# Optimization experiments

Hardware: AMD Instinct MI355X
Metric: run time of the kernel (lower is better)

## Reference

```python
import jax, jax.numpy as jnp
import numpy as np

N_NODES = 50000
N_EDGES = 1600000
IN_DIM = 6
H = 64


def _sage_conv(x, src, dst, W_l, b_l, W_r, num_nodes):
    """PyG SAGEConv (aggr='mean'): out = lin_l(mean_{j in N(i)} x_j) + lin_r(x_i).
    lin_l has bias, lin_r has no bias (PyG default)."""
    # mean-aggregate neighbor features at destination nodes
    agg = jax.ops.segment_sum(x[src], dst, num_segments=num_nodes)          # [N, d]
    cnt = jax.ops.segment_sum(jnp.ones((src.shape[0],), x.dtype), dst,
                              num_segments=num_nodes)                        # [N]
    mean = agg / jnp.maximum(cnt, 1.0)[:, None]
    return mean @ W_l + b_l + x @ W_r


def setup_inputs() -> dict:
    key = jax.random.key(0)
    ks = jax.random.split(key, 8)
    x = jax.random.normal(ks[0], (N_NODES, IN_DIM), dtype=jnp.float32)
    edge_index = jax.random.randint(ks[1], (2, N_EDGES), 0, N_NODES, dtype=jnp.int64)
    # Kaiming-ish scaled params
    def lin(k, fan_in, fan_out):
        return jax.random.normal(k, (fan_in, fan_out), dtype=jnp.float32) / np.sqrt(fan_in)
    return {
        "x": x,
        "edge_index": edge_index,
        "W1_l": lin(ks[2], IN_DIM, H),
        "b1_l": jnp.zeros((H,), jnp.float32),
        "W1_r": lin(ks[3], IN_DIM, H),
        "W2_l": lin(ks[4], H, H),
        "b2_l": jnp.zeros((H,), jnp.float32),
        "W2_r": lin(ks[5], H, H),
    }


def reference(x, edge_index, W1_l, b1_l, W1_r, W2_l, b2_l, W2_r):
    src, dst = edge_index[0], edge_index[1]
    n = x.shape[0]
    z = jax.nn.relu(_sage_conv(x, src, dst, W1_l, b1_l, W1_r, n))  # [N, H]
    z = _sage_conv(z, src, dst, W2_l, b2_l, W2_r, n)               # [N, H]
    return z
```

## Files before the change

### kernel.cpp

```cpp
#include <hip/hip_runtime.h>

#define N_NODES 50000
#define N_EDGES 1600000
#define IN_DIM 6
#define H 64

#define NBUCKET 196
#define NBLK 196
#define EPB 8192
#define BCAP 9216

#define L2PAD 72

__device__ __forceinline__ float bf2f(unsigned short u) {
    return __uint_as_float(((unsigned int)u) << 16);
}
__device__ __forceinline__ unsigned short f2bf(float f) {
    unsigned int u = __float_as_uint(f);
    u += 0x7fffu + ((u >> 16) & 1u);
    return (unsigned short)(u >> 16);
}

__global__ __launch_bounds__(512) void scatter_bucketed(
        const int* __restrict__ ei,
        const float* __restrict__ x,
        int* __restrict__ gcur,
        unsigned int* __restrict__ ebin,
        const float* __restrict__ W2l,
        const float* __restrict__ W2r,
        unsigned short* __restrict__ Wlt,
        unsigned short* __restrict__ Wrt,
        unsigned short* __restrict__ z,
        float* __restrict__ xp) {
    int t = threadIdx.x;
    int gid = blockIdx.x * 512 + t;
    if (gid < N_NODES) {
        const float2* xr = (const float2*)(x + (size_t)gid * IN_DIM);
        float2 p0 = xr[0], p1 = xr[1], p2 = xr[2];
        float4* xw = (float4*)(xp + ((size_t)gid << 3));
        xw[0] = make_float4(p0.x, p0.y, p1.x, p1.y);
        xw[1] = make_float4(p2.x, p2.y, 0.f, 0.f);
    }
    if (blockIdx.x == NBLK) {
        for (int i = t; i < H * H; i += 512) {
            int k = i >> 6, f = i & 63;
            Wlt[f * H + k] = f2bf(W2l[i]);
            Wrt[f * H + k] = f2bf(W2r[i]);
        }
        if (t < H) z[(size_t)N_NODES * H + t] = 0;
        return;
    }
    __shared__ unsigned int sedge[EPB];
    __shared__ int hist[NBUCKET];
    __shared__ int cur[NBUCKET];
    for (int i = t; i < NBUCKET; i += 512) hist[i] = 0;
    __syncthreads();
    int e0 = blockIdx.x * EPB;
    int cnt = min(EPB, N_EDGES - e0);
    const int4* s4 = (const int4*)(ei + e0);
    const int4* d4 = (const int4*)(ei + N_EDGES + e0);
    for (int k = t; k * 4 < cnt; k += 512) {
        int4 sv = s4[k];
        int4 dv = d4[k];
        sedge[k * 4 + 0] = ((unsigned)sv.x << 16) | (unsigned)dv.x;
        sedge[k * 4 + 1] = ((unsigned)sv.y << 16) | (unsigned)dv.y;
        sedge[k * 4 + 2] = ((unsigned)sv.z << 16) | (unsigned)dv.z;
        sedge[k * 4 + 3] = ((unsigned)sv.w << 16) | (unsigned)dv.w;
        atomicAdd(&hist[dv.x >> 8], 1);
        atomicAdd(&hist[dv.y >> 8], 1);
        atomicAdd(&hist[dv.z >> 8], 1);
        atomicAdd(&hist[dv.w >> 8], 1);
    }
    __syncthreads();
    for (int i = t; i < NBUCKET; i += 512)
        cur[i] = atomicAdd(&gcur[i], hist[i]);
    __syncthreads();
    for (int k = t; k * 4 < cnt; k += 512) {
#pragma unroll
        for (int j = 0; j < 4; j++) {
            unsigned int p = sedge[k * 4 + j];
            int b = (int)(p & 0xffffu) >> 8;
            int pos = atomicAdd(&cur[b], 1);
            if (pos < BCAP) ebin[(size_t)b * BCAP + pos] = p;
        }
    }
}

__global__ __launch_bounds__(1024) void bucket_layer1(
        const unsigned int* __restrict__ ebin,
        const int* __restrict__ gcur,
        const float* __restrict__ xp,
        const float* __restrict__ W1l,
        const float* __restrict__ b1,
        const float* __restrict__ W1r,
        int2* __restrict__ rowpair,
        unsigned short* __restrict__ esrc,
        unsigned short* __restrict__ z) {
    __shared__ int raw[BCAP];
    __shared__ unsigned short ssrc[BCAP];
    __shared__ int sdeg[256];
    __shared__ int sstart[256];
    __shared__ int scur[256];
    __shared__ int wsum[4];
    __shared__ float sW1l[IN_DIM * H];
    __shared__ float sW1r[IN_DIM * H];
    float* smx   = (float*)raw;
    float* spart = (float*)raw + 4096;

    int t = threadIdx.x;
    int lane = t & 63, w = t >> 6;
    int b = blockIdx.x;
    int base = b << 8;
    int nn = min(256, N_NODES - base);
    int ebase = b * BCAP;
    int cnt = min(gcur[b], BCAP);

    if (t < 256) sdeg[t] = 0;
    if (t < IN_DIM * H) { sW1l[t] = W1l[t]; sW1r[t] = W1r[t]; }
    for (int i = t; i < cnt; i += 1024) raw[i] = (int)ebin[ebase + i];
    __syncthreads();
    for (int i = t; i < cnt; i += 1024) atomicAdd(&sdeg[raw[i] & 0xff], 1);
    __syncthreads();
    int v = 0, s = 0;
    if (t < 256) {
        v = sdeg[t]; s = v;
#pragma unroll
        for (int off = 1; off < 64; off <<= 1) {
            int u = __shfl_up(s, off);
            if (lane >= off) s += u;
        }
        if (lane == 63) wsum[w] = s;
    }
    __syncthreads();
    if (t < 256) {
        int woff = 0;
        for (int k = 0; k < w; k++) woff += wsum[k];
        int excl = s - v + woff;
        sstart[t] = excl;
        scur[t] = excl;
        if (t < nn) rowpair[base + t] = make_int2(ebase + excl, ebase + excl + v);
    }
    __syncthreads();
    for (int i = t; i < cnt; i += 1024) {
        int p = raw[i];
        int pos = atomicAdd(&scur[p & 0xff], 1);
        ssrc[pos] = (unsigned short)((unsigned)p >> 16);
    }
    __syncthreads();
    for (int i = t; i < cnt; i += 1024)
        esrc[ebase + i] = ssrc[i];
    for (int i = t; i < nn * 8; i += 1024) {
        int node = i >> 3, k = i & 7;
        if (k < 6) smx[node * 16 + 6 + k] = xp[(size_t)(base + node) * 8 + k];
    }

    int node = t & 255, q = t >> 8;
    float a0 = 0.f, a1 = 0.f, a2 = 0.f, a3 = 0.f, a4 = 0.f, a5 = 0.f;
    int deg = 0, st = 0;
    if (node < nn) { deg = sdeg[node]; st = sstart[node]; }
    for (int i = st + q; i < st + deg; i += 4) {
        int src = ssrc[i];
        const float4* xs = (const float4*)(xp + ((size_t)src << 3));
        float4 p0 = xs[0], p1 = xs[1];
        a0 += p0.x; a1 += p0.y; a2 += p0.z;
        a3 += p0.w; a4 += p1.x; a5 += p1.y;
    }
    if (q > 0 && node < nn) {
        float* sp = &spart[(q - 1) * (256 * 6) + node * 6];
        sp[0] = a0; sp[1] = a1; sp[2] = a2; sp[3] = a3; sp[4] = a4; sp[5] = a5;
    }
    __syncthreads();
    if (q == 0 && node < nn) {
        float inv = 1.0f / fmaxf((float)deg, 1.0f);
        const float* p1p = &spart[0 * (256 * 6) + node * 6];
        const float* p2p = &spart[1 * (256 * 6) + node * 6];
        const float* p3p = &spart[2 * (256 * 6) + node * 6];
        smx[node * 16 + 0] = (a0 + p1p[0] + p2p[0] + p3p[0]) * inv;
        smx[node * 16 + 1] = (a1 + p1p[1] + p2p[1] + p3p[1]) * inv;
        smx[node * 16 + 2] = (a2 + p1p[2] + p2p[2] + p3p[2]) * inv;
        smx[node * 16 + 3] = (a3 + p1p[3] + p2p[3] + p3p[3]) * inv;
        smx[node * 16 + 4] = (a4 + p1p[4] + p2p[4] + p3p[4]) * inv;
        smx[node * 16 + 5] = (a5 + p1p[5] + p2p[5] + p3p[5]) * inv;
    }
    __syncthreads();

    int feat = t & 63, ng = t >> 6;
    float wl[IN_DIM], wr[IN_DIM];
#pragma unroll
    for (int k = 0; k < IN_DIM; k++) { wl[k] = sW1l[k * H + feat]; wr[k] = sW1r[k * H + feat]; }
    float bias = b1[feat];
    for (int nb = ng; nb < nn; nb += 16) {
        const float4* row = (const float4*)&smx[nb * 16];
        float4 r0 = row[0], r1 = row[1], r2 = row[2];
        float acc = bias;
        acc += r0.x * wl[0] + r0.y * wl[1] + r0.z * wl[2]
             + r0.w * wl[3] + r1.x * wl[4] + r1.y * wl[5];
        acc += r1.z * wr[0] + r1.w * wr[1] + r2.x * wr[2]
             + r2.y * wr[3] + r2.z * wr[4] + r2.w * wr[5];
        z[(size_t)(base + nb) * H + feat] = f2bf(fmaxf(acc, 0.0f));
    }
}

__global__ __launch_bounds__(512) void layer2_mfma(
        const unsigned short* __restrict__ zin,
        const int2* __restrict__ rowpair,
        const unsigned short* __restrict__ esrc,
        const unsigned short* __restrict__ Wlt,
        const float* __restrict__ b2,
        const unsigned short* __restrict__ Wrt,
        float* __restrict__ out) {
    typedef short bf16x8 __attribute__((ext_vector_type(8)));
    typedef float f32x4 __attribute__((ext_vector_type(4)));
    __shared__ __attribute__((aligned(16))) unsigned short smean[32 * L2PAD];
    __shared__ __attribute__((aligned(16))) unsigned short szl[32 * L2PAD];
    __shared__ __attribute__((aligned(16))) unsigned short sWl[64 * L2PAD];
    __shared__ __attribute__((aligned(16))) unsigned short sWr[64 * L2PAD];

    int t = threadIdx.x;
    int w = t >> 6, lane = t & 63;
    int g = lane >> 4, lg = lane & 15;
    int n0 = blockIdx.x * 32;

    {
        const ushort4* wl4 = (const ushort4*)Wlt;
        const ushort4* wr4 = (const ushort4*)Wrt;
        for (int qi = t; qi < H * H / 4; qi += 512) {
            int f = qi >> 4, kq = qi & 15;
            *(ushort4*)&sWl[f * L2PAD + kq * 4] = wl4[qi];
            *(ushort4*)&sWr[f * L2PAD + kq * 4] = wr4[qi];
        }
    }

    for (int q = 0; q < 4; q++) {
        int ln = w * 4 + q;
        int n = n0 + ln;
        bool valid = (n < N_NODES);
        int r0 = 0, r1 = 0;
        if (valid) { int2 rp = rowpair[n]; r0 = rp.x; r1 = rp.y; }
        float4 acc = make_float4(0.f, 0.f, 0.f, 0.f);
        for (int base = r0; base < r1; base += 64) {
            int ii = base + lane;
            int idx = (ii < r1) ? (int)esrc[ii] : N_NODES;
            int rem = r1 - base;
#pragma unroll
            for (int tt = 0; tt < 8; tt++) {
                int s = __shfl(idx, tt * 4 + g);
                const ushort4* zr = (const ushort4*)(zin + (size_t)s * H);
                ushort4 vv = zr[lg];
                acc.x += bf2f(vv.x); acc.y += bf2f(vv.y);
                acc.z += bf2f(vv.z); acc.w += bf2f(vv.w);
            }
            if (rem > 32) {
#pragma unroll
                for (int tt = 8; tt < 16; tt++) {
                    int s = __shfl(idx, tt * 4 + g);
                    const ushort4* zr = (const ushort4*)(zin + (size_t)s * H);
                    ushort4 vv = zr[lg];
                    acc.x += bf2f(vv.x); acc.y += bf2f(vv.y);
                    acc.z += bf2f(vv.z); acc.w += bf2f(vv.w);
                }
            }
        }
#pragma unroll
        for (int off = 16; off < 64; off <<= 1) {
            acc.x += __shfl_xor(acc.x, off);
            acc.y += __shfl_xor(acc.y, off);
            acc.z += __shfl_xor(acc.z, off);
            acc.w += __shfl_xor(acc.w, off);
        }
        float inv = 1.0f / fmaxf((float)(r1 - r0), 1.0f);
        if (g == 0) {
            ushort4 mb;
            mb.x = f2bf(acc.x * inv); mb.y = f2bf(acc.y * inv);
            mb.z = f2bf(acc.z * inv); mb.w = f2bf(acc.w * inv);
            *(ushort4*)&smean[ln * L2PAD + lg * 4] = mb;
        }
        int nz = valid ? n : N_NODES;
        szl[ln * L2PAD + lane] = zin[(size_t)nz * H + lane];
    }
    __syncthreads();

    int nb = w >> 2, fb = w & 3;
    f32x4 acc = {0.f, 0.f, 0.f, 0.f};
#pragma unroll
    for (int ks = 0; ks < 2; ks++) {
        int ko = ks * 32 + g * 8;
        bf16x8 aM = *(const bf16x8*)&smean[(nb * 16 + lg) * L2PAD + ko];
        bf16x8 aZ = *(const bf16x8*)&szl[(nb * 16 + lg) * L2PAD + ko];
        bf16x8 bL = *(const bf16x8*)&sWl[(fb * 16 + lg) * L2PAD + ko];
        bf16x8 bR = *(const bf16x8*)&sWr[(fb * 16 + lg) * L2PAD + ko];
        acc = __builtin_amdgcn_mfma_f32_16x16x32_bf16(aM, bL, acc, 0, 0, 0);
        acc = __builtin_amdgcn_mfma_f32_16x16x32_bf16(aZ, bR, acc, 0, 0, 0);
    }
    float bias = b2[fb * 16 + lg];
#pragma unroll
    for (int r = 0; r < 4; r++) {
        int node = n0 + nb * 16 + g * 4 + r;
        if (node < N_NODES)
            out[(size_t)node * H + fb * 16 + lg] = acc[r] + bias;
    }
}

extern "C" void kernel_launch(void* const* d_in, const int* in_sizes, int n_in,
                              void* d_out, int out_size, void* d_ws, size_t ws_size,
                              hipStream_t stream) {
    const float* x   = (const float*)d_in[0];
    const int*   ei  = (const int*)d_in[1];
    const float* W1l = (const float*)d_in[2];
    const float* b1  = (const float*)d_in[3];
    const float* W1r = (const float*)d_in[4];
    const float* W2l = (const float*)d_in[5];
    const float* b2  = (const float*)d_in[6];
    const float* W2r = (const float*)d_in[7];
    float* out = (float*)d_out;

    int* gcur = (int*)d_ws;
    int2* rowpair = (int2*)(gcur + 208);
    unsigned int*   ebin = (unsigned int*)(rowpair + N_NODES);
    unsigned short* esrc = (unsigned short*)(ebin + (size_t)NBUCKET * BCAP);
    unsigned short* z    = esrc + (size_t)NBUCKET * BCAP;
    unsigned short* Wlt  = z + (size_t)(N_NODES + 1) * H;
    unsigned short* Wrt  = Wlt + H * H;
    float* xp = (float*)(Wrt + H * H);

    hipMemsetAsync(gcur, 0, NBUCKET * sizeof(int), stream);

    scatter_bucketed<<<NBLK + 1, 512, 0, stream>>>(ei, x, gcur, ebin,
                                                   W2l, W2r, Wlt, Wrt, z, xp);
    bucket_layer1<<<NBUCKET, 1024, 0, stream>>>(ebin, gcur, xp, W1l, b1, W1r,
                                                rowpair, esrc, z);
    layer2_mfma<<<(N_NODES + 31) / 32, 512, 0, stream>>>(z, rowpair, esrc,
                                                         Wlt, b2, Wrt, out);
}
```

Measured before the change: 151.8 us.

## Split layer-1 activations into two 32-feature planes for cache-friendly layer-2 gather

Stores the bf16 hidden activations z as two planes of 32 features each instead of one 64-wide row per node. The layer-2 kernel then runs two passes, gathering 64-byte half rows from one plane at a time, which shrinks the working set touched per pass so it fits better in L2/MALL. The cost is twice as many gather passes, shuffles and index loads, and each gathered segment is half as wide.

```diff
diff --git a/kernel.cpp b/kernel.cpp
--- a/kernel.cpp
+++ b/kernel.cpp
@@ -11,6 +11,7 @@
 #define BCAP 9216
 
 #define L2PAD 72
+#define ZPLANE ((size_t)(N_NODES + 1) * 32)
 
 __device__ __forceinline__ float bf2f(unsigned short u) {
     return __uint_as_float(((unsigned int)u) << 16);
@@ -47,7 +48,8 @@
             Wlt[f * H + k] = f2bf(W2l[i]);
             Wrt[f * H + k] = f2bf(W2r[i]);
         }
-        if (t < H) z[(size_t)N_NODES * H + t] = 0;
+        if (t < 64)
+            z[(size_t)(t >> 5) * ZPLANE + (size_t)N_NODES * 32 + (t & 31)] = 0;
         return;
     }
     __shared__ unsigned int sedge[EPB];
@@ -189,6 +191,8 @@
 #pragma unroll
     for (int k = 0; k < IN_DIM; k++) { wl[k] = sW1l[k * H + feat]; wr[k] = sW1r[k * H + feat]; }
     float bias = b1[feat];
+    int plane = feat >> 5, f5 = feat & 31;
+    unsigned short* zw = z + (size_t)plane * ZPLANE + f5;
     for (int nb = ng; nb < nn; nb += 16) {
         const float4* row = (const float4*)&smx[nb * 16];
         float4 r0 = row[0], r1 = row[1], r2 = row[2];
@@ -197,7 +201,7 @@
              + r0.w * wl[3] + r1.x * wl[4] + r1.y * wl[5];
         acc += r1.z * wr[0] + r1.w * wr[1] + r2.x * wr[2]
              + r2.y * wr[3] + r2.z * wr[4] + r2.w * wr[5];
-        z[(size_t)(base + nb) * H + feat] = f2bf(fmaxf(acc, 0.0f));
+        zw[(size_t)(base + nb) * 32] = f2bf(fmaxf(acc, 0.0f));
     }
 }
 
@@ -218,7 +222,7 @@
 
     int t = threadIdx.x;
     int w = t >> 6, lane = t & 63;
-    int g = lane >> 4, lg = lane & 15;
+    int g8 = lane >> 3, l8 = lane & 7;
     int n0 = blockIdx.x * 32;
 
     {
@@ -231,55 +235,63 @@
         }
     }
 
-    for (int q = 0; q < 4; q++) {
-        int ln = w * 4 + q;
-        int n = n0 + ln;
-        bool valid = (n < N_NODES);
-        int r0 = 0, r1 = 0;
-        if (valid) { int2 rp = rowpair[n]; r0 = rp.x; r1 = rp.y; }
-        float4 acc = make_float4(0.f, 0.f, 0.f, 0.f);
-        for (int base = r0; base < r1; base += 64) {
-            int ii = base + lane;
-            int idx = (ii < r1) ? (int)esrc[ii] : N_NODES;
-            int rem = r1 - base;
-#pragma unroll
-            for (int tt = 0; tt < 8; tt++) {
-                int s = __shfl(idx, tt * 4 + g);
-                const ushort4* zr = (const ushort4*)(zin + (size_t)s * H);
-                ushort4 vv = zr[lg];
-                acc.x += bf2f(vv.x); acc.y += bf2f(vv.y);
-                acc.z += bf2f(vv.z); acc.w += bf2f(vv.w);
-            }
-            if (rem > 32) {
-#pragma unroll
-                for (int tt = 8; tt < 16; tt++) {
-                    int s = __shfl(idx, tt * 4 + g);
-                    const ushort4* zr = (const ushort4*)(zin + (size_t)s * H);
-                    ushort4 vv = zr[lg];
+#pragma unroll 1
+    for (int pass = 0; pass < 2; pass++) {
+        const unsigned short* zp = zin + (size_t)pass * ZPLANE;
+        for (int q = 0; q < 4; q++) {
+            int ln = w * 4 + q;
+            int n = n0 + ln;
+            bool valid = (n < N_NODES);
+            int r0 = 0, r1 = 0;
+            if (valid) { int2 rp = rowpair[n]; r0 = rp.x; r1 = rp.y; }
+            float4 acc = make_float4(0.f, 0.f, 0.f, 0.f);
+            for (int base = r0; base < r1; base += 64) {
+                int ii = base + lane;
+                int idx = (ii < r1) ? (int)esrc[ii] : N_NODES;
+                int rem = r1 - base;
+#pragma unroll
+                for (int tt = 0; tt < 4; tt++) {
+                    int s = __shfl(idx, tt * 8 + g8);
+                    const ushort4* zr = (const ushort4*)(zp + (size_t)s * 32);
+                    ushort4 vv = zr[l8];
                     acc.x += bf2f(vv.x); acc.y += bf2f(vv.y);
                     acc.z += bf2f(vv.z); acc.w += bf2f(vv.w);
                 }
+                if (rem > 32) {
+#pragma unroll
+                    for (int tt = 4; tt < 8; tt++) {
+                        int s = __shfl(idx, tt * 8 + g8);
+                        const ushort4* zr = (const ushort4*)(zp + (size_t)s * 32);
+                        ushort4 vv = zr[l8];
+                        acc.x += bf2f(vv.x); acc.y += bf2f(vv.y);
+                        acc.z += bf2f(vv.z); acc.w += bf2f(vv.w);
+                    }
+                }
             }
-        }
-#pragma unroll
-        for (int off = 16; off < 64; off <<= 1) {
-            acc.x += __shfl_xor(acc.x, off);
-            acc.y += __shfl_xor(acc.y, off);
-            acc.z += __shfl_xor(acc.z, off);
-            acc.w += __shfl_xor(acc.w, off);
-        }
-        float inv = 1.0f / fmaxf((float)(r1 - r0), 1.0f);
-        if (g == 0) {
-            ushort4 mb;
-            mb.x = f2bf(acc.x * inv); mb.y = f2bf(acc.y * inv);
-            mb.z = f2bf(acc.z * inv); mb.w = f2bf(acc.w * inv);
-            *(ushort4*)&smean[ln * L2PAD + lg * 4] = mb;
-        }
-        int nz = valid ? n : N_NODES;
-        szl[ln * L2PAD + lane] = zin[(size_t)nz * H + lane];
-    }
-    __syncthreads();
-
+#pragma unroll
+            for (int off = 8; off < 64; off <<= 1) {
+                acc.x += __shfl_xor(acc.x, off);
+                acc.y += __shfl_xor(acc.y, off);
+                acc.z += __shfl_xor(acc.z, off);
+                acc.w += __shfl_xor(acc.w, off);
+            }
+            float inv = 1.0f / fmaxf((float)(r1 - r0), 1.0f);
+            if (g8 == 0) {
+                ushort4 mb;
+                mb.x = f2bf(acc.x * inv); mb.y = f2bf(acc.y * inv);
+                mb.z = f2bf(acc.z * inv); mb.w = f2bf(acc.w * inv);
+                *(ushort4*)&smean[ln * L2PAD + pass * 32 + l8 * 4] = mb;
+            }
+            if (pass == 0) {
+                int nz = valid ? n : N_NODES;
+                szl[ln * L2PAD + lane] =
+                    zin[(size_t)(lane >> 5) * ZPLANE + (size_t)nz * 32 + (lane & 31)];
+            }
+        }
+    }
+    __syncthreads();
+
+    int g = lane >> 4, lg = lane & 15;
     int nb = w >> 2, fb = w & 3;
     f32x4 acc = {0.f, 0.f, 0.f, 0.f};
 #pragma unroll
@@ -319,7 +331,7 @@
     unsigned int*   ebin = (unsigned int*)(rowpair + N_NODES);
     unsigned short* esrc = (unsigned short*)(ebin + (size_t)NBUCKET * BCAP);
     unsigned short* z    = esrc + (size_t)NBUCKET * BCAP;
-    unsigned short* Wlt  = z + (size_t)(N_NODES + 1) * H;
+    unsigned short* Wlt  = z + 2 * ZPLANE;
     unsigned short* Wrt  = Wlt + H * H;
     float* xp = (float*)(Wrt + H * H);
 
```

New measurement: 154.3 us. No clear change (+1.6%).
